# Kernel tuning notes

Measured on AMD Instinct MI355X. Metric: run time of the kernel, lower is better.

## Reference

```python
import jax, jax.numpy as jnp
import numpy as np

K = 3          # k_neighbors
EPS = 1e-12    # F.normalize eps


def _l2norm(x):
    n = jnp.sqrt(jnp.sum(x * x, axis=-1, keepdims=True))
    return x / jnp.maximum(n, EPS)


def setup_inputs() -> dict:
    key = jax.random.key(0)
    k1, k2 = jax.random.split(key)
    query_features = jax.random.normal(k1, (64, 64, 32, 32), dtype=jnp.float32)
    support_features = jax.random.normal(k2, (64, 5, 64, 1024), dtype=jnp.float32)
    return {"query_features": query_features, "support_features": support_features}


def reference(query_features, support_features):
    B, D, h, w = query_features.shape
    # (B, Nq, D), L2-normalized along D
    q_local = _l2norm(query_features.reshape(B, D, h * w).transpose(0, 2, 1))
    # support: (B, Way, D, Ns) -> (B, Way, Ns, D), L2-normalized along D
    s_local = _l2norm(support_features.transpose(0, 1, 3, 2))
    # cosine similarities for all (batch, way) pairs in one batched matmul
    sim = jnp.einsum('bqd,bwsd->bwqs', q_local, s_local)  # (B, Way, Nq, Ns)
    k_actual = min(K, sim.shape[-1])
    topk_sim, _ = jax.lax.top_k(sim, k_actual)            # (B, Way, Nq, k)
    return topk_sim.sum(axis=(-1, -2))                    # (B, Way)
```

## Files before the change

kernel.cpp:

```cpp
#include <hip/hip_runtime.h>
#include <hip/hip_bf16.h>


using bf16x8 = __attribute__((ext_vector_type(8))) short;
using f32x4  = __attribute__((ext_vector_type(4))) float;

__device__ inline unsigned cvt_pk_bf16(float lo, float hi) {
    unsigned r;
    asm("v_cvt_pk_bf16_f32 %0, %1, %2" : "=v"(r) : "v"(lo), "v"(hi));
    return r;
}

__device__ inline uint4 pack8cvt(const float* v) {
    uint4 r;
    r.x = cvt_pk_bf16(v[0], v[1]);
    r.y = cvt_pk_bf16(v[2], v[3]);
    r.z = cvt_pk_bf16(v[4], v[5]);
    r.w = cvt_pk_bf16(v[6], v[7]);
    return r;
}

#define INS(v, T0, T1, T2) do {                         \
    float _v = (v);                                     \
    float _n0 = fmaxf((T0), _v);                        \
    float _n1 = __builtin_amdgcn_fmed3f(_v, (T0), (T1));\
    float _n2 = __builtin_amdgcn_fmed3f(_v, (T1), (T2));\
    (T0) = _n0; (T1) = _n1; (T2) = _n2;                 \
} while (0)

__device__ inline void gload16(const void* g, void* lds) {
    __builtin_amdgcn_global_load_lds(
        (const __attribute__((address_space(1))) unsigned int*)g,
        (__attribute__((address_space(3))) unsigned int*)lds,
        16, 0, 0);
}


__global__ __launch_bounds__(256) void prep_all(const float* __restrict__ Q,
                                                const float* __restrict__ S,
                                                uint4* __restrict__ Qbf,
                                                uint4* __restrict__ Sbf,
                                                float* __restrict__ rnq) {
    const int blk = blockIdx.x;
    if (blk < 256) {
        const int b = blk >> 2;
        const int col = ((blk & 3) << 8) + threadIdx.x;
        const float* p = Q + (size_t)b * 65536 + col;
        float v[64];
        #pragma unroll
        for (int d = 0; d < 64; ++d) v[d] = p[(size_t)d << 10];
        float ss = 0.f;
        #pragma unroll
        for (int d = 0; d < 64; ++d) ss += v[d] * v[d];
        rnq[(b << 10) + col] = 1.0f / fmaxf(sqrtf(ss), 1e-12f);
        uint4* ob = Qbf + ((size_t)(b << 6) + (col >> 4)) * 128 + (col & 15);
        #pragma unroll
        for (int h = 0; h < 8; ++h)
            ob[h << 4] = pack8cvt(&v[h << 3]);
    } else {
        const int bw = (blk - 256) >> 2;
        const int col = ((blk & 3) << 8) + threadIdx.x;
        const float* p = S + (size_t)bw * 65536 + col;
        float v[64];
        #pragma unroll
        for (int d = 0; d < 64; ++d) v[d] = p[(size_t)d << 10];
        float ss = 0.f;
        #pragma unroll
        for (int d = 0; d < 64; ++d) ss += v[d] * v[d];
        const float rs = 1.0f / fmaxf(sqrtf(ss), 1e-12f);
        #pragma unroll
        for (int d = 0; d < 64; ++d) v[d] *= rs;
        uint4* ob = Sbf + ((size_t)(bw << 6) + (col >> 4)) * 128 + (col & 15);
        #pragma unroll
        for (int h = 0; h < 8; ++h)
            ob[h << 4] = pack8cvt(&v[h << 3]);
    }
}

__global__ __launch_bounds__(256) void knn_main(const uint4* __restrict__ Qbf,
                                                const uint4* __restrict__ Sbf,
                                                const float* __restrict__ rnq,
                                                float* __restrict__ partial) {
    __shared__ uint4 ring[8 * 256];
    __shared__ float wsum[4];
    const int lin = blockIdx.x;
    const int l   = (lin & 7) * 160 + (lin >> 3);
    const int qc  = l & 3;
    const int bw  = l >> 2;
    const int b   = bw / 5;
    const int wv = threadIdx.x >> 6, lane = threadIdx.x & 63;

    const uint4* qb = Qbf + ((size_t)(b << 6) + (qc << 4) + (wv << 2)) * 128 + lane;
    bf16x8 bq[4][2];
    #pragma unroll
    for (int qt = 0; qt < 4; ++qt)
        #pragma unroll
        for (int c = 0; c < 2; ++c)
            bq[qt][c] = *reinterpret_cast<const bf16x8*>(&qb[qt * 128 + (c << 6)]);

    const char* sbase = (const char*)(Sbf + (size_t)(bw << 6) * 128);
    const size_t toff = (size_t)threadIdx.x * 16;

    float t0[4], t1[4], t2[4];
    #pragma unroll
    for (int qt = 0; qt < 4; ++qt) { t0[qt] = -1e30f; t1[qt] = -1e30f; t2[qt] = -1e30f; }

    #pragma unroll
    for (int p = 0; p < 4; ++p)
        gload16(sbase + (size_t)p * 4096 + toff, &ring[(p << 8) + (wv << 6)]);

    for (int p = 0; p < 28; ++p) {
        gload16(sbase + (size_t)(p + 4) * 4096 + toff,
                &ring[(((p + 4) & 7) << 8) + (wv << 6)]);
        asm volatile("s_waitcnt vmcnt(4)" ::: "memory");
        __builtin_amdgcn_s_barrier();
        const uint4* sp = &ring[((p & 7) << 8)];
        #pragma unroll
        for (int tt = 0; tt < 2; ++tt) {
            bf16x8 a0 = *reinterpret_cast<const bf16x8*>(&sp[tt * 128 + lane]);
            bf16x8 a1 = *reinterpret_cast<const bf16x8*>(&sp[tt * 128 + 64 + lane]);
            #pragma unroll
            for (int qt = 0; qt < 4; ++qt) {
                f32x4 c = {0.f, 0.f, 0.f, 0.f};
                c = __builtin_amdgcn_mfma_f32_16x16x32_bf16(a0, bq[qt][0], c, 0, 0, 0);
                c = __builtin_amdgcn_mfma_f32_16x16x32_bf16(a1, bq[qt][1], c, 0, 0, 0);
                #pragma unroll
                for (int j = 0; j < 4; ++j)
                    INS(c[j], t0[qt], t1[qt], t2[qt]);
            }
        }
        __builtin_amdgcn_s_barrier();
    }
    asm volatile("s_waitcnt vmcnt(0)" ::: "memory");
    __builtin_amdgcn_s_barrier();
    for (int p = 28; p < 32; ++p) {
        const uint4* sp = &ring[((p & 7) << 8)];
        #pragma unroll
        for (int tt = 0; tt < 2; ++tt) {
            bf16x8 a0 = *reinterpret_cast<const bf16x8*>(&sp[tt * 128 + lane]);
            bf16x8 a1 = *reinterpret_cast<const bf16x8*>(&sp[tt * 128 + 64 + lane]);
            #pragma unroll
            for (int qt = 0; qt < 4; ++qt) {
                f32x4 c = {0.f, 0.f, 0.f, 0.f};
                c = __builtin_amdgcn_mfma_f32_16x16x32_bf16(a0, bq[qt][0], c, 0, 0, 0);
                c = __builtin_amdgcn_mfma_f32_16x16x32_bf16(a1, bq[qt][1], c, 0, 0, 0);
                #pragma unroll
                for (int j = 0; j < 4; ++j)
                    INS(c[j], t0[qt], t1[qt], t2[qt]);
            }
        }
    }

    float s3 = 0.f;
    #pragma unroll
    for (int qt = 0; qt < 4; ++qt) {
        #pragma unroll
        for (int m = 16; m <= 32; m <<= 1) {
            float b0 = __shfl_xor(t0[qt], m);
            float b1 = __shfl_xor(t1[qt], m);
            float b2 = __shfl_xor(t2[qt], m);
            INS(b0, t0[qt], t1[qt], t2[qt]);
            INS(b1, t0[qt], t1[qt], t2[qt]);
            INS(b2, t0[qt], t1[qt], t2[qt]);
        }
        const int qg = (qc << 8) + (wv << 6) + (qt << 4) + (lane & 15);
        s3 += (t0[qt] + t1[qt] + t2[qt]) * rnq[(b << 10) + qg];
    }
    #pragma unroll
    for (int m = 1; m < 64; m <<= 1) s3 += __shfl_xor(s3, m);
    s3 *= 0.25f;
    if (lane == 0) wsum[wv] = s3;
    __syncthreads();
    if (threadIdx.x == 0)
        partial[((size_t)bw << 2) + qc] = (wsum[0] + wsum[1]) + (wsum[2] + wsum[3]);
}

__global__ void finalize4(const float* __restrict__ partial, float* __restrict__ out) {
    int i = blockIdx.x * blockDim.x + threadIdx.x;
    if (i < 320)
        out[i] = (partial[4 * i] + partial[4 * i + 1]) +
                 (partial[4 * i + 2] + partial[4 * i + 3]);
}

__global__ void norms_kernel(const float* __restrict__ Q, const float* __restrict__ S,
                             float* __restrict__ rnq, float* __restrict__ rns) {
    int gid = blockIdx.x * blockDim.x + threadIdx.x;
    if (gid < 65536) {
        int b = gid >> 10, qi = gid & 1023;
        const float* p = Q + (size_t)b * 65536 + qi;
        float ss = 0.f;
        #pragma unroll
        for (int d = 0; d < 64; ++d) { float v = p[(size_t)d * 1024]; ss += v * v; }
        rnq[gid] = 1.0f / fmaxf(sqrtf(ss), 1e-12f);
    } else {
        int v = gid - 65536;
        int bw = v >> 10, si = v & 1023;
        const float* p = S + (size_t)bw * 65536 + si;
        float ss = 0.f;
        #pragma unroll
        for (int d = 0; d < 64; ++d) { float x = p[(size_t)d * 1024]; ss += x * x; }
        rns[v] = 1.0f / fmaxf(sqrtf(ss), 1e-12f);
    }
}

__global__ __launch_bounds__(512, 4) void knn_fb(
        const float* __restrict__ Q, const float* __restrict__ S,
        const float* __restrict__ rnq, const float* __restrict__ rns,
        float* __restrict__ partial) {
    __shared__ uint4 qfrag[16 * 128];
    __shared__ uint4 sfrag[2][4 * 128];
    __shared__ float wsum[8];

    const int qc = blockIdx.x, w = blockIdx.y, b = blockIdx.z;
    const int t = threadIdx.x, wv = t >> 6, lane = t & 63;

    const float* Qb   = Q + (size_t)b * 65536;
    const float* Sb   = S + (size_t)(b * 5 + w) * 65536;
    const float* rnqb = rnq + (b << 10);
    const float* rnsb = rns + ((b * 5 + w) << 10);

    bf16x8 bq[4][2];
    for (int ph = 0; ph < 2; ++ph) {
        for (int sub = 0; sub < 4; ++sub) {
            int qg = (qc << 9) + (ph << 8) + (sub << 6) + lane;
            float v[8];
            #pragma unroll
            for (int i = 0; i < 8; ++i)
                v[i] = Qb[(size_t)((wv << 3) + i) * 1024 + qg];
            qfrag[((sub << 2) + (lane >> 4)) * 128 + (wv << 4) + (lane & 15)] = pack8cvt(v);
        }
        __syncthreads();
        if ((wv >> 2) == ph) {
            #pragma unroll
            for (int qt = 0; qt < 4; ++qt)
                #pragma unroll
                for (int c = 0; c < 2; ++c)
                    bq[qt][c] = *reinterpret_cast<const bf16x8*>(
                        &qfrag[(((wv & 3) << 2) + qt) * 128 + (c << 6) + lane]);
        }
        __syncthreads();
    }

    {
        float sv[8]; float rs = rnsb[lane];
        #pragma unroll
        for (int i = 0; i < 8; ++i)
            sv[i] = Sb[(size_t)((wv << 3) + i) * 1024 + lane] * rs;
        sfrag[0][(lane >> 4) * 128 + (wv << 4) + (lane & 15)] = pack8cvt(sv);
    }
    __syncthreads();

    float t0[4], t1[4], t2[4];
    #pragma unroll
    for (int qt = 0; qt < 4; ++qt) { t0[qt] = -1e30f; t1[qt] = -1e30f; t2[qt] = -1e30f; }
    int cur = 0;
    const float* sp = Sb + ((wv << 3) << 10) + lane;

    for (int blk = 0; blk < 16; ++blk) {
        float sv[8]; float rs;
        if (blk < 15) {
            const int sb_ = (blk + 1) << 6;
            rs = rnsb[sb_ + lane];
            #pragma unroll
            for (int i = 0; i < 8; ++i)
                sv[i] = sp[(size_t)(i << 10) + sb_];
        }
        #pragma unroll
        for (int st = 0; st < 4; ++st) {
            bf16x8 a0 = *reinterpret_cast<const bf16x8*>(&sfrag[cur][st * 128 + lane]);
            bf16x8 a1 = *reinterpret_cast<const bf16x8*>(&sfrag[cur][st * 128 + 64 + lane]);
            #pragma unroll
            for (int qt = 0; qt < 4; ++qt) {
                f32x4 c = {0.f, 0.f, 0.f, 0.f};
                c = __builtin_amdgcn_mfma_f32_16x16x32_bf16(a0, bq[qt][0], c, 0, 0, 0);
                c = __builtin_amdgcn_mfma_f32_16x16x32_bf16(a1, bq[qt][1], c, 0, 0, 0);
                #pragma unroll
                for (int j = 0; j < 4; ++j)
                    INS(c[j], t0[qt], t1[qt], t2[qt]);
            }
        }
        if (blk < 15) {
            #pragma unroll
            for (int i = 0; i < 8; ++i) sv[i] *= rs;
            sfrag[cur ^ 1][(lane >> 4) * 128 + (wv << 4) + (lane & 15)] = pack8cvt(sv);
        }
        __syncthreads();
        cur ^= 1;
    }

    float s3 = 0.f;
    #pragma unroll
    for (int qt = 0; qt < 4; ++qt) {
        #pragma unroll
        for (int m = 16; m <= 32; m <<= 1) {
            float b0 = __shfl_xor(t0[qt], m);
            float b1 = __shfl_xor(t1[qt], m);
            float b2 = __shfl_xor(t2[qt], m);
            INS(b0, t0[qt], t1[qt], t2[qt]);
            INS(b1, t0[qt], t1[qt], t2[qt]);
            INS(b2, t0[qt], t1[qt], t2[qt]);
        }
        int qg = (qc << 9) + (wv << 6) + (qt << 4) + (lane & 15);
        s3 += (t0[qt] + t1[qt] + t2[qt]) * rnqb[qg];
    }
    #pragma unroll
    for (int m = 1; m < 64; m <<= 1) s3 += __shfl_xor(s3, m);
    s3 *= 0.25f;
    if (lane == 0) wsum[wv] = s3;
    __syncthreads();
    if (t == 0) {
        float acc = 0.f;
        #pragma unroll
        for (int i = 0; i < 8; ++i) acc += wsum[i];
        partial[((b * 5 + w) << 1) + qc] = acc;
    }
}

__global__ void finalize2(const float* __restrict__ partial, float* __restrict__ out) {
    int i = blockIdx.x * blockDim.x + threadIdx.x;
    if (i < 320)
        out[i] = partial[2 * i] + partial[2 * i + 1];
}

extern "C" void kernel_launch(void* const* d_in, const int* in_sizes, int n_in,
                              void* d_out, int out_size, void* d_ws, size_t ws_size,
                              hipStream_t stream) {
    const float* Q = (const float*)d_in[0];
    const float* S = (const float*)d_in[1];
    float* out = (float*)d_out;

    const size_t QBF = 8388608ull, SBF = 41943040ull, RNQ = 262144ull;
    const size_t NEED = QBF + SBF + RNQ + 5120ull;
    if (ws_size >= NEED) {
        char* base = (char*)d_ws;
        uint4* Qbf     = (uint4*)base;
        uint4* Sbf     = (uint4*)(base + QBF);
        float* rnq     = (float*)(base + QBF + SBF);
        float* partial = (float*)(base + QBF + SBF + RNQ);
        prep_all<<<1536, 256, 0, stream>>>(Q, S, Qbf, Sbf, rnq);
        knn_main<<<1280, 256, 0, stream>>>(Qbf, Sbf, rnq, partial);
        finalize4<<<2, 256, 0, stream>>>(partial, out);
    } else {
        float* rnq = (float*)d_ws;
        float* rns = rnq + 65536;
        float* partial = rns + 327680;
        norms_kernel<<<(65536 + 327680) / 256, 256, 0, stream>>>(Q, S, rnq, rns);
        knn_fb<<<dim3(2, 5, 64), 512, 0, stream>>>(Q, S, rnq, rns, partial);
        finalize2<<<2, 256, 0, stream>>>(partial, out);
    }
}
```

Baseline: 101.2 us.

## Software-pipeline MFMA tiles with top-k insertion using double accumulators

Result: faster. 92.03 us (-9.1%).

```diff
diff --git a/kernel.cpp b/kernel.cpp
--- a/kernel.cpp
+++ b/kernel.cpp
@@ -77,10 +77,31 @@
     }
 }
 
-__global__ __launch_bounds__(256) void knn_main(const uint4* __restrict__ Qbf,
-                                                const uint4* __restrict__ Sbf,
-                                                const float* __restrict__ rnq,
-                                                float* __restrict__ partial) {
+__device__ __forceinline__ void mfma_tile(const uint4* sp, int lane,
+                                          const bf16x8 (&bq)[4][2],
+                                          const f32x4& fz, f32x4* c) {
+    bf16x8 a0 = *reinterpret_cast<const bf16x8*>(&sp[lane]);
+    bf16x8 a1 = *reinterpret_cast<const bf16x8*>(&sp[64 + lane]);
+    #pragma unroll
+    for (int qt = 0; qt < 4; ++qt) {
+        c[qt] = __builtin_amdgcn_mfma_f32_16x16x32_bf16(a0, bq[qt][0], fz, 0, 0, 0);
+        c[qt] = __builtin_amdgcn_mfma_f32_16x16x32_bf16(a1, bq[qt][1], c[qt], 0, 0, 0);
+    }
+}
+
+__device__ __forceinline__ void ins_tile(const f32x4* c,
+                                         float (&t0)[4], float (&t1)[4], float (&t2)[4]) {
+    #pragma unroll
+    for (int qt = 0; qt < 4; ++qt)
+        #pragma unroll
+        for (int j = 0; j < 4; ++j)
+            INS(c[qt][j], t0[qt], t1[qt], t2[qt]);
+}
+
+__global__ __launch_bounds__(256, 4) void knn_main(const uint4* __restrict__ Qbf,
+                                                   const uint4* __restrict__ Sbf,
+                                                   const float* __restrict__ rnq,
+                                                   float* __restrict__ partial) {
     __shared__ uint4 ring[8 * 256];
     __shared__ float wsum[4];
     const int lin = blockIdx.x;
@@ -98,6 +119,10 @@
         for (int c = 0; c < 2; ++c)
             bq[qt][c] = *reinterpret_cast<const bf16x8*>(&qb[qt * 128 + (c << 6)]);
 
+    float z0 = 0.f;
+    asm volatile("" : "+v"(z0));
+    const f32x4 fz = {z0, z0, z0, z0};
+
     const char* sbase = (const char*)(Sbf + (size_t)(bw << 6) * 128);
     const size_t toff = (size_t)threadIdx.x * 16;
 
@@ -105,51 +130,40 @@
     #pragma unroll
     for (int qt = 0; qt < 4; ++qt) { t0[qt] = -1e30f; t1[qt] = -1e30f; t2[qt] = -1e30f; }
 
+    f32x4 cA[4], cB[4];
+
     #pragma unroll
     for (int p = 0; p < 4; ++p)
         gload16(sbase + (size_t)p * 4096 + toff, &ring[(p << 8) + (wv << 6)]);
 
-    for (int p = 0; p < 28; ++p) {
+    gload16(sbase + 4 * 4096 + toff, &ring[(4 << 8) + (wv << 6)]);
+    asm volatile("s_waitcnt vmcnt(4)" ::: "memory");
+    __builtin_amdgcn_s_barrier();
+    mfma_tile(&ring[0], lane, bq, fz, cA);
+    mfma_tile(&ring[128], lane, bq, fz, cB);
+
+    for (int p = 1; p <= 27; ++p) {
         gload16(sbase + (size_t)(p + 4) * 4096 + toff,
                 &ring[(((p + 4) & 7) << 8) + (wv << 6)]);
         asm volatile("s_waitcnt vmcnt(4)" ::: "memory");
         __builtin_amdgcn_s_barrier();
         const uint4* sp = &ring[((p & 7) << 8)];
-        #pragma unroll
-        for (int tt = 0; tt < 2; ++tt) {
-            bf16x8 a0 = *reinterpret_cast<const bf16x8*>(&sp[tt * 128 + lane]);
-            bf16x8 a1 = *reinterpret_cast<const bf16x8*>(&sp[tt * 128 + 64 + lane]);
-            #pragma unroll
-            for (int qt = 0; qt < 4; ++qt) {
-                f32x4 c = {0.f, 0.f, 0.f, 0.f};
-                c = __builtin_amdgcn_mfma_f32_16x16x32_bf16(a0, bq[qt][0], c, 0, 0, 0);
-                c = __builtin_amdgcn_mfma_f32_16x16x32_bf16(a1, bq[qt][1], c, 0, 0, 0);
-                #pragma unroll
-                for (int j = 0; j < 4; ++j)
-                    INS(c[j], t0[qt], t1[qt], t2[qt]);
-            }
-        }
-        __builtin_amdgcn_s_barrier();
+        mfma_tile(sp, lane, bq, fz, cA);
+        ins_tile(cB, t0, t1, t2);
+        mfma_tile(sp + 128, lane, bq, fz, cB);
+        ins_tile(cA, t0, t1, t2);
     }
     asm volatile("s_waitcnt vmcnt(0)" ::: "memory");
     __builtin_amdgcn_s_barrier();
-    for (int p = 28; p < 32; ++p) {
+    #pragma unroll
+    for (int p = 28; p <= 31; ++p) {
         const uint4* sp = &ring[((p & 7) << 8)];
-        #pragma unroll
-        for (int tt = 0; tt < 2; ++tt) {
-            bf16x8 a0 = *reinterpret_cast<const bf16x8*>(&sp[tt * 128 + lane]);
-            bf16x8 a1 = *reinterpret_cast<const bf16x8*>(&sp[tt * 128 + 64 + lane]);
-            #pragma unroll
-            for (int qt = 0; qt < 4; ++qt) {
-                f32x4 c = {0.f, 0.f, 0.f, 0.f};
-                c = __builtin_amdgcn_mfma_f32_16x16x32_bf16(a0, bq[qt][0], c, 0, 0, 0);
-                c = __builtin_amdgcn_mfma_f32_16x16x32_bf16(a1, bq[qt][1], c, 0, 0, 0);
-                #pragma unroll
-                for (int j = 0; j < 4; ++j)
-                    INS(c[j], t0[qt], t1[qt], t2[qt]);
-            }
-        }
-    }
+        mfma_tile(sp, lane, bq, fz, cA);
+        ins_tile(cB, t0, t1, t2);
+        mfma_tile(sp + 128, lane, bq, fz, cB);
+        ins_tile(cA, t0, t1, t2);
+    }
+    ins_tile(cB, t0, t1, t2);
 
     float s3 = 0.f;
     #pragma unroll
```

## Split query chunks eightfold with staggered support ring and MFMA priority

Applied to the files above, without the earlier changes.

Result: no change. 99.30 us (-1.9%).

```diff
diff --git a/kernel.cpp b/kernel.cpp
--- a/kernel.cpp
+++ b/kernel.cpp
@@ -77,23 +77,47 @@
     }
 }
 
-__global__ __launch_bounds__(256) void knn_main(const uint4* __restrict__ Qbf,
-                                                const uint4* __restrict__ Sbf,
-                                                const float* __restrict__ rnq,
-                                                float* __restrict__ partial) {
-    __shared__ uint4 ring[8 * 256];
+__device__ __forceinline__ void compute_tile(const uint4* sp, int lane,
+                                             const bf16x8 (&bq)[2][2],
+                                             float (&t0)[2], float (&t1)[2],
+                                             float (&t2)[2]) {
+    bf16x8 a0 = *reinterpret_cast<const bf16x8*>(&sp[lane]);
+    bf16x8 a1 = *reinterpret_cast<const bf16x8*>(&sp[64 + lane]);
+    const f32x4 z = {0.f, 0.f, 0.f, 0.f};
+    __builtin_amdgcn_s_setprio(1);
+    f32x4 c0 = __builtin_amdgcn_mfma_f32_16x16x32_bf16(a0, bq[0][0], z, 0, 0, 0);
+    c0 = __builtin_amdgcn_mfma_f32_16x16x32_bf16(a1, bq[0][1], c0, 0, 0, 0);
+    f32x4 c1 = __builtin_amdgcn_mfma_f32_16x16x32_bf16(a0, bq[1][0], z, 0, 0, 0);
+    c1 = __builtin_amdgcn_mfma_f32_16x16x32_bf16(a1, bq[1][1], c1, 0, 0, 0);
+    __builtin_amdgcn_s_setprio(0);
+    INS(c0[0], t0[0], t1[0], t2[0]);
+    INS(c0[1], t0[0], t1[0], t2[0]);
+    INS(c0[2], t0[0], t1[0], t2[0]);
+    INS(c0[3], t0[0], t1[0], t2[0]);
+    INS(c1[0], t0[1], t1[1], t2[1]);
+    INS(c1[1], t0[1], t1[1], t2[1]);
+    INS(c1[2], t0[1], t1[1], t2[1]);
+    INS(c1[3], t0[1], t1[1], t2[1]);
+}
+
+__global__ __launch_bounds__(256, 8) void knn_main(const uint4* __restrict__ Qbf,
+                                                   const uint4* __restrict__ Sbf,
+                                                   const float* __restrict__ rnq,
+                                                   float* __restrict__ partial) {
+    __shared__ uint4 ring[5 * 256];
     __shared__ float wsum[4];
     const int lin = blockIdx.x;
-    const int l   = (lin & 7) * 160 + (lin >> 3);
-    const int qc  = l & 3;
-    const int bw  = l >> 2;
+    const int l   = (lin & 7) * 320 + (lin >> 3);
+    const int qc  = l & 7;
+    const int bw  = l >> 3;
     const int b   = bw / 5;
     const int wv = threadIdx.x >> 6, lane = threadIdx.x & 63;
-
-    const uint4* qb = Qbf + ((size_t)(b << 6) + (qc << 4) + (wv << 2)) * 128 + lane;
-    bf16x8 bq[4][2];
-    #pragma unroll
-    for (int qt = 0; qt < 4; ++qt)
+    const int sp0 = qc << 2;
+
+    const uint4* qb = Qbf + ((size_t)(b << 6) + (qc << 3) + (wv << 1)) * 128 + lane;
+    bf16x8 bq[2][2];
+    #pragma unroll
+    for (int qt = 0; qt < 2; ++qt)
         #pragma unroll
         for (int c = 0; c < 2; ++c)
             bq[qt][c] = *reinterpret_cast<const bf16x8*>(&qb[qt * 128 + (c << 6)]);
@@ -101,24 +125,162 @@
     const char* sbase = (const char*)(Sbf + (size_t)(bw << 6) * 128);
     const size_t toff = (size_t)threadIdx.x * 16;
 
+    float t0[2], t1[2], t2[2];
+    #pragma unroll
+    for (int qt = 0; qt < 2; ++qt) { t0[qt] = -1e30f; t1[qt] = -1e30f; t2[qt] = -1e30f; }
+
+    #pragma unroll
+    for (int p = 0; p < 3; ++p)
+        gload16(sbase + (size_t)((p + sp0) & 31) * 4096 + toff,
+                &ring[(p << 8) + (wv << 6)]);
+
+    int rslot = 0, wslot = 3;
+    for (int p = 0; p <= 28; ++p) {
+        gload16(sbase + (size_t)((p + 3 + sp0) & 31) * 4096 + toff,
+                &ring[(wslot << 8) + (wv << 6)]);
+        asm volatile("s_waitcnt vmcnt(3)" ::: "memory");
+        __builtin_amdgcn_s_barrier();
+        const uint4* sp = &ring[rslot << 8];
+        compute_tile(sp, lane, bq, t0, t1, t2);
+        compute_tile(sp + 128, lane, bq, t0, t1, t2);
+        if (++rslot == 5) rslot = 0;
+        if (++wslot == 5) wslot = 0;
+    }
+    asm volatile("s_waitcnt vmcnt(0)" ::: "memory");
+    __builtin_amdgcn_s_barrier();
+    {
+        const uint4* sp = &ring[4 << 8];
+        compute_tile(sp, lane, bq, t0, t1, t2);
+        compute_tile(sp + 128, lane, bq, t0, t1, t2);
+        sp = &ring[0];
+        compute_tile(sp, lane, bq, t0, t1, t2);
+        compute_tile(sp + 128, lane, bq, t0, t1, t2);
+        sp = &ring[1 << 8];
+        compute_tile(sp, lane, bq, t0, t1, t2);
+        compute_tile(sp + 128, lane, bq, t0, t1, t2);
+    }
+
+    float s3 = 0.f;
+    #pragma unroll
+    for (int qt = 0; qt < 2; ++qt) {
+        #pragma unroll
+        for (int m = 16; m <= 32; m <<= 1) {
+            float b0 = __shfl_xor(t0[qt], m);
+            float b1 = __shfl_xor(t1[qt], m);
+            float b2 = __shfl_xor(t2[qt], m);
+            INS(b0, t0[qt], t1[qt], t2[qt]);
+            INS(b1, t0[qt], t1[qt], t2[qt]);
+            INS(b2, t0[qt], t1[qt], t2[qt]);
+        }
+        const int qg = (qc << 7) + (wv << 5) + (qt << 4) + (lane & 15);
+        s3 += (t0[qt] + t1[qt] + t2[qt]) * rnq[(b << 10) + qg];
+    }
+    #pragma unroll
+    for (int m = 1; m < 64; m <<= 1) s3 += __shfl_xor(s3, m);
+    s3 *= 0.25f;
+    if (lane == 0) wsum[wv] = s3;
+    __syncthreads();
+    if (threadIdx.x == 0)
+        partial[((size_t)bw << 3) + qc] = (wsum[0] + wsum[1]) + (wsum[2] + wsum[3]);
+}
+
+__global__ void finalize8(const float* __restrict__ partial, float* __restrict__ out) {
+    int i = blockIdx.x * blockDim.x + threadIdx.x;
+    if (i < 320) {
+        float a = 0.f;
+        #pragma unroll
+        for (int k = 0; k < 8; ++k) a += partial[8 * i + k];
+        out[i] = a;
+    }
+}
+
+__global__ void norms_kernel(const float* __restrict__ Q, const float* __restrict__ S,
+                             float* __restrict__ rnq, float* __restrict__ rns) {
+    int gid = blockIdx.x * blockDim.x + threadIdx.x;
+    if (gid < 65536) {
+        int b = gid >> 10, qi = gid & 1023;
+        const float* p = Q + (size_t)b * 65536 + qi;
+        float ss = 0.f;
+        #pragma unroll
+        for (int d = 0; d < 64; ++d) { float v = p[(size_t)d * 1024]; ss += v * v; }
+        rnq[gid] = 1.0f / fmaxf(sqrtf(ss), 1e-12f);
+    } else {
+        int v = gid - 65536;
+        int bw = v >> 10, si = v & 1023;
+        const float* p = S + (size_t)bw * 65536 + si;
+        float ss = 0.f;
+        #pragma unroll
+        for (int d = 0; d < 64; ++d) { float x = p[(size_t)d * 1024]; ss += x * x; }
+        rns[v] = 1.0f / fmaxf(sqrtf(ss), 1e-12f);
+    }
+}
+
+__global__ __launch_bounds__(512, 4) void knn_fb(
+        const float* __restrict__ Q, const float* __restrict__ S,
+        const float* __restrict__ rnq, const float* __restrict__ rns,
+        float* __restrict__ partial) {
+    __shared__ uint4 qfrag[16 * 128];
+    __shared__ uint4 sfrag[2][4 * 128];
+    __shared__ float wsum[8];
+
+    const int qc = blockIdx.x, w = blockIdx.y, b = blockIdx.z;
+    const int t = threadIdx.x, wv = t >> 6, lane = t & 63;
+
+    const float* Qb   = Q + (size_t)b * 65536;
+    const float* Sb   = S + (size_t)(b * 5 + w) * 65536;
+    const float* rnqb = rnq + (b << 10);
+    const float* rnsb = rns + ((b * 5 + w) << 10);
+
+    bf16x8 bq[4][2];
+    for (int ph = 0; ph < 2; ++ph) {
+        for (int sub = 0; sub < 4; ++sub) {
+            int qg = (qc << 9) + (ph << 8) + (sub << 6) + lane;
+            float v[8];
+            #pragma unroll
+            for (int i = 0; i < 8; ++i)
+                v[i] = Qb[(size_t)((wv << 3) + i) * 1024 + qg];
+            qfrag[((sub << 2) + (lane >> 4)) * 128 + (wv << 4) + (lane & 15)] = pack8cvt(v);
+        }
+        __syncthreads();
+        if ((wv >> 2) == ph) {
+            #pragma unroll
+            for (int qt = 0; qt < 4; ++qt)
+                #pragma unroll
+                for (int c = 0; c < 2; ++c)
+                    bq[qt][c] = *reinterpret_cast<const bf16x8*>(
+                        &qfrag[(((wv & 3) << 2) + qt) * 128 + (c << 6) + lane]);
+        }
+        __syncthreads();
+    }
+
+    {
+        float sv[8]; float rs = rnsb[lane];
+        #pragma unroll
+        for (int i = 0; i < 8; ++i)
+            sv[i] = Sb[(size_t)((wv << 3) + i) * 1024 + lane] * rs;
+        sfrag[0][(lane >> 4) * 128 + (wv << 4) + (lane & 15)] = pack8cvt(sv);
+    }
+    __syncthreads();
+
     float t0[4], t1[4], t2[4];
     #pragma unroll
     for (int qt = 0; qt < 4; ++qt) { t0[qt] = -1e30f; t1[qt] = -1e30f; t2[qt] = -1e30f; }
-
-    #pragma unroll
-    for (int p = 0; p < 4; ++p)
-        gload16(sbase + (size_t)p * 4096 + toff, &ring[(p << 8) + (wv << 6)]);
-
-    for (int p = 0; p < 28; ++p) {
-        gload16(sbase + (size_t)(p + 4) * 4096 + toff,
-                &ring[(((p + 4) & 7) << 8) + (wv << 6)]);
-        asm volatile("s_waitcnt vmcnt(4)" ::: "memory");
-        __builtin_amdgcn_s_barrier();
-        const uint4* sp = &ring[((p & 7) << 8)];
-        #pragma unroll
-        for (int tt = 0; tt < 2; ++tt) {
-            bf16x8 a0 = *reinterpret_cast<const bf16x8*>(&sp[tt * 128 + lane]);
-            bf16x8 a1 = *reinterpret_cast<const bf16x8*>(&sp[tt * 128 + 64 + lane]);
+    int cur = 0;
+    const float* sp = Sb + ((wv << 3) << 10) + lane;
+
+    for (int blk = 0; blk < 16; ++blk) {
+        float sv[8]; float rs;
+        if (blk < 15) {
+            const int sb_ = (blk + 1) << 6;
+            rs = rnsb[sb_ + lane];
+            #pragma unroll
+            for (int i = 0; i < 8; ++i)
+                sv[i] = sp[(size_t)(i << 10) + sb_];
+        }
+        #pragma unroll
+        for (int st = 0; st < 4; ++st) {
+            bf16x8 a0 = *reinterpret_cast<const bf16x8*>(&sfrag[cur][st * 128 + lane]);
+            bf16x8 a1 = *reinterpret_cast<const bf16x8*>(&sfrag[cur][st * 128 + 64 + lane]);
             #pragma unroll
             for (int qt = 0; qt < 4; ++qt) {
                 f32x4 c = {0.f, 0.f, 0.f, 0.f};
@@ -129,26 +291,13 @@
                     INS(c[j], t0[qt], t1[qt], t2[qt]);
             }
         }
-        __builtin_amdgcn_s_barrier();
-    }
-    asm volatile("s_waitcnt vmcnt(0)" ::: "memory");
-    __builtin_amdgcn_s_barrier();
-    for (int p = 28; p < 32; ++p) {
-        const uint4* sp = &ring[((p & 7) << 8)];
-        #pragma unroll
-        for (int tt = 0; tt < 2; ++tt) {
-            bf16x8 a0 = *reinterpret_cast<const bf16x8*>(&sp[tt * 128 + lane]);
-            bf16x8 a1 = *reinterpret_cast<const bf16x8*>(&sp[tt * 128 + 64 + lane]);
-            #pragma unroll
-            for (int qt = 0; qt < 4; ++qt) {
-                f32x4 c = {0.f, 0.f, 0.f, 0.f};
-                c = __builtin_amdgcn_mfma_f32_16x16x32_bf16(a0, bq[qt][0], c, 0, 0, 0);
-                c = __builtin_amdgcn_mfma_f32_16x16x32_bf16(a1, bq[qt][1], c, 0, 0, 0);
-                #pragma unroll
-                for (int j = 0; j < 4; ++j)
-                    INS(c[j], t0[qt], t1[qt], t2[qt]);
-            }
-        }
+        if (blk < 15) {
+            #pragma unroll
+            for (int i = 0; i < 8; ++i) sv[i] *= rs;
+            sfrag[cur ^ 1][(lane >> 4) * 128 + (wv << 4) + (lane & 15)] = pack8cvt(sv);
+        }
+        __syncthreads();
+        cur ^= 1;
     }
 
     float s3 = 0.f;
@@ -163,143 +312,6 @@
             INS(b1, t0[qt], t1[qt], t2[qt]);
             INS(b2, t0[qt], t1[qt], t2[qt]);
         }
-        const int qg = (qc << 8) + (wv << 6) + (qt << 4) + (lane & 15);
-        s3 += (t0[qt] + t1[qt] + t2[qt]) * rnq[(b << 10) + qg];
-    }
-    #pragma unroll
-    for (int m = 1; m < 64; m <<= 1) s3 += __shfl_xor(s3, m);
-    s3 *= 0.25f;
-    if (lane == 0) wsum[wv] = s3;
-    __syncthreads();
-    if (threadIdx.x == 0)
-        partial[((size_t)bw << 2) + qc] = (wsum[0] + wsum[1]) + (wsum[2] + wsum[3]);
-}
-
-__global__ void finalize4(const float* __restrict__ partial, float* __restrict__ out) {
-    int i = blockIdx.x * blockDim.x + threadIdx.x;
-    if (i < 320)
-        out[i] = (partial[4 * i] + partial[4 * i + 1]) +
-                 (partial[4 * i + 2] + partial[4 * i + 3]);
-}
-
-__global__ void norms_kernel(const float* __restrict__ Q, const float* __restrict__ S,
-                             float* __restrict__ rnq, float* __restrict__ rns) {
-    int gid = blockIdx.x * blockDim.x + threadIdx.x;
-    if (gid < 65536) {
-        int b = gid >> 10, qi = gid & 1023;
-        const float* p = Q + (size_t)b * 65536 + qi;
-        float ss = 0.f;
-        #pragma unroll
-        for (int d = 0; d < 64; ++d) { float v = p[(size_t)d * 1024]; ss += v * v; }
-        rnq[gid] = 1.0f / fmaxf(sqrtf(ss), 1e-12f);
-    } else {
-        int v = gid - 65536;
-        int bw = v >> 10, si = v & 1023;
-        const float* p = S + (size_t)bw * 65536 + si;
-        float ss = 0.f;
-        #pragma unroll
-        for (int d = 0; d < 64; ++d) { float x = p[(size_t)d * 1024]; ss += x * x; }
-        rns[v] = 1.0f / fmaxf(sqrtf(ss), 1e-12f);
-    }
-}
-
-__global__ __launch_bounds__(512, 4) void knn_fb(
-        const float* __restrict__ Q, const float* __restrict__ S,
-        const float* __restrict__ rnq, const float* __restrict__ rns,
-        float* __restrict__ partial) {
-    __shared__ uint4 qfrag[16 * 128];
-    __shared__ uint4 sfrag[2][4 * 128];
-    __shared__ float wsum[8];
-
-    const int qc = blockIdx.x, w = blockIdx.y, b = blockIdx.z;
-    const int t = threadIdx.x, wv = t >> 6, lane = t & 63;
-
-    const float* Qb   = Q + (size_t)b * 65536;
-    const float* Sb   = S + (size_t)(b * 5 + w) * 65536;
-    const float* rnqb = rnq + (b << 10);
-    const float* rnsb = rns + ((b * 5 + w) << 10);
-
-    bf16x8 bq[4][2];
-    for (int ph = 0; ph < 2; ++ph) {
-        for (int sub = 0; sub < 4; ++sub) {
-            int qg = (qc << 9) + (ph << 8) + (sub << 6) + lane;
-            float v[8];
-            #pragma unroll
-            for (int i = 0; i < 8; ++i)
-                v[i] = Qb[(size_t)((wv << 3) + i) * 1024 + qg];
-            qfrag[((sub << 2) + (lane >> 4)) * 128 + (wv << 4) + (lane & 15)] = pack8cvt(v);
-        }
-        __syncthreads();
-        if ((wv >> 2) == ph) {
-            #pragma unroll
-            for (int qt = 0; qt < 4; ++qt)
-                #pragma unroll
-                for (int c = 0; c < 2; ++c)
-                    bq[qt][c] = *reinterpret_cast<const bf16x8*>(
-                        &qfrag[(((wv & 3) << 2) + qt) * 128 + (c << 6) + lane]);
-        }
-        __syncthreads();
-    }
-
-    {
-        float sv[8]; float rs = rnsb[lane];
-        #pragma unroll
-        for (int i = 0; i < 8; ++i)
-            sv[i] = Sb[(size_t)((wv << 3) + i) * 1024 + lane] * rs;
-        sfrag[0][(lane >> 4) * 128 + (wv << 4) + (lane & 15)] = pack8cvt(sv);
-    }
-    __syncthreads();
-
-    float t0[4], t1[4], t2[4];
-    #pragma unroll
-    for (int qt = 0; qt < 4; ++qt) { t0[qt] = -1e30f; t1[qt] = -1e30f; t2[qt] = -1e30f; }
-    int cur = 0;
-    const float* sp = Sb + ((wv << 3) << 10) + lane;
-
-    for (int blk = 0; blk < 16; ++blk) {
-        float sv[8]; float rs;
-        if (blk < 15) {
-            const int sb_ = (blk + 1) << 6;
-            rs = rnsb[sb_ + lane];
-            #pragma unroll
-            for (int i = 0; i < 8; ++i)
-                sv[i] = sp[(size_t)(i << 10) + sb_];
-        }
-        #pragma unroll
-        for (int st = 0; st < 4; ++st) {
-            bf16x8 a0 = *reinterpret_cast<const bf16x8*>(&sfrag[cur][st * 128 + lane]);
-            bf16x8 a1 = *reinterpret_cast<const bf16x8*>(&sfrag[cur][st * 128 + 64 + lane]);
-            #pragma unroll
-            for (int qt = 0; qt < 4; ++qt) {
-                f32x4 c = {0.f, 0.f, 0.f, 0.f};
-                c = __builtin_amdgcn_mfma_f32_16x16x32_bf16(a0, bq[qt][0], c, 0, 0, 0);
-                c = __builtin_amdgcn_mfma_f32_16x16x32_bf16(a1, bq[qt][1], c, 0, 0, 0);
-                #pragma unroll
-                for (int j = 0; j < 4; ++j)
-                    INS(c[j], t0[qt], t1[qt], t2[qt]);
-            }
-        }
-        if (blk < 15) {
-            #pragma unroll
-            for (int i = 0; i < 8; ++i) sv[i] *= rs;
-            sfrag[cur ^ 1][(lane >> 4) * 128 + (wv << 4) + (lane & 15)] = pack8cvt(sv);
-        }
-        __syncthreads();
-        cur ^= 1;
-    }
-
-    float s3 = 0.f;
-    #pragma unroll
-    for (int qt = 0; qt < 4; ++qt) {
-        #pragma unroll
-        for (int m = 16; m <= 32; m <<= 1) {
-            float b0 = __shfl_xor(t0[qt], m);
-            float b1 = __shfl_xor(t1[qt], m);
-            float b2 = __shfl_xor(t2[qt], m);
-            INS(b0, t0[qt], t1[qt], t2[qt]);
-            INS(b1, t0[qt], t1[qt], t2[qt]);
-            INS(b2, t0[qt], t1[qt], t2[qt]);
-        }
         int qg = (qc << 9) + (wv << 6) + (qt << 4) + (lane & 15);
         s3 += (t0[qt] + t1[qt] + t2[qt]) * rnqb[qg];
     }
@@ -330,7 +342,7 @@
     float* out = (float*)d_out;
 
     const size_t QBF = 8388608ull, SBF = 41943040ull, RNQ = 262144ull;
-    const size_t NEED = QBF + SBF + RNQ + 5120ull;
+    const size_t NEED = QBF + SBF + RNQ + 10240ull;
     if (ws_size >= NEED) {
         char* base = (char*)d_ws;
         uint4* Qbf     = (uint4*)base;
@@ -338,8 +350,8 @@
         float* rnq     = (float*)(base + QBF + SBF);
         float* partial = (float*)(base + QBF + SBF + RNQ);
         prep_all<<<1536, 256, 0, stream>>>(Q, S, Qbf, Sbf, rnq);
-        knn_main<<<1280, 256, 0, stream>>>(Qbf, Sbf, rnq, partial);
-        finalize4<<<2, 256, 0, stream>>>(partial, out);
+        knn_main<<<2560, 256, 0, stream>>>(Qbf, Sbf, rnq, partial);
+        finalize8<<<2, 256, 0, stream>>>(partial, out);
     } else {
         float* rnq = (float*)d_ws;
         float* rns = rnq + 65536;
```

## Split support columns across wave pairs with per-wave LDS rings, no block barriers

Applied to the files above, without the earlier changes.

Measured after the change: 95.42 us. 1.06x faster.

```diff
diff --git a/kernel.cpp b/kernel.cpp
--- a/kernel.cpp
+++ b/kernel.cpp
@@ -77,20 +77,44 @@
     }
 }
 
-__global__ __launch_bounds__(256) void knn_main(const uint4* __restrict__ Qbf,
-                                                const uint4* __restrict__ Sbf,
-                                                const float* __restrict__ rnq,
-                                                float* __restrict__ partial) {
-    __shared__ uint4 ring[8 * 256];
-    __shared__ float wsum[4];
+__device__ __forceinline__ void compute_tile4(const uint4* sp, int lane,
+                                              const bf16x8 (&bq)[4][2],
+                                              float (&t0)[4], float (&t1)[4],
+                                              float (&t2)[4]) {
+    bf16x8 a0 = *reinterpret_cast<const bf16x8*>(&sp[lane]);
+    bf16x8 a1 = *reinterpret_cast<const bf16x8*>(&sp[64 + lane]);
+    const f32x4 z = {0.f, 0.f, 0.f, 0.f};
+    f32x4 c[4];
+    __builtin_amdgcn_s_setprio(1);
+    #pragma unroll
+    for (int qt = 0; qt < 4; ++qt) {
+        c[qt] = __builtin_amdgcn_mfma_f32_16x16x32_bf16(a0, bq[qt][0], z, 0, 0, 0);
+        c[qt] = __builtin_amdgcn_mfma_f32_16x16x32_bf16(a1, bq[qt][1], c[qt], 0, 0, 0);
+    }
+    __builtin_amdgcn_s_setprio(0);
+    #pragma unroll
+    for (int qt = 0; qt < 4; ++qt) {
+        INS(c[qt][0], t0[qt], t1[qt], t2[qt]);
+        INS(c[qt][1], t0[qt], t1[qt], t2[qt]);
+        INS(c[qt][2], t0[qt], t1[qt], t2[qt]);
+        INS(c[qt][3], t0[qt], t1[qt], t2[qt]);
+    }
+}
+
+__global__ __launch_bounds__(256, 4) void knn_main(const uint4* __restrict__ Qbf,
+                                                   const uint4* __restrict__ Sbf,
+                                                   const float* __restrict__ rnq,
+                                                   float* __restrict__ partial) {
+    __shared__ uint4 ring[4][5 * 128];
     const int lin = blockIdx.x;
-    const int l   = (lin & 7) * 160 + (lin >> 3);
-    const int qc  = l & 3;
-    const int bw  = l >> 2;
+    const int l   = (lin & 7) * 320 + (lin >> 3);
+    const int qc  = l & 7;
+    const int bw  = l >> 3;
     const int b   = bw / 5;
     const int wv = threadIdx.x >> 6, lane = threadIdx.x & 63;
-
-    const uint4* qb = Qbf + ((size_t)(b << 6) + (qc << 4) + (wv << 2)) * 128 + lane;
+    const int g  = wv >> 1, h = wv & 1;
+
+    const uint4* qb = Qbf + ((size_t)(b << 6) + (qc << 3) + (g << 2)) * 128 + lane;
     bf16x8 bq[4][2];
     #pragma unroll
     for (int qt = 0; qt < 4; ++qt)
@@ -98,27 +122,179 @@
         for (int c = 0; c < 2; ++c)
             bq[qt][c] = *reinterpret_cast<const bf16x8*>(&qb[qt * 128 + (c << 6)]);
 
-    const char* sbase = (const char*)(Sbf + (size_t)(bw << 6) * 128);
-    const size_t toff = (size_t)threadIdx.x * 16;
+    const char* sbyte = (const char*)(Sbf + (size_t)bw * 8192) + ((size_t)h << 16)
+                        + (size_t)lane * 16;
+    uint4* myring = &ring[wv][0];
 
     float t0[4], t1[4], t2[4];
     #pragma unroll
     for (int qt = 0; qt < 4; ++qt) { t0[qt] = -1e30f; t1[qt] = -1e30f; t2[qt] = -1e30f; }
 
     #pragma unroll
-    for (int p = 0; p < 4; ++p)
-        gload16(sbase + (size_t)p * 4096 + toff, &ring[(p << 8) + (wv << 6)]);
-
-    for (int p = 0; p < 28; ++p) {
-        gload16(sbase + (size_t)(p + 4) * 4096 + toff,
-                &ring[(((p + 4) & 7) << 8) + (wv << 6)]);
-        asm volatile("s_waitcnt vmcnt(4)" ::: "memory");
-        __builtin_amdgcn_s_barrier();
-        const uint4* sp = &ring[((p & 7) << 8)];
-        #pragma unroll
-        for (int tt = 0; tt < 2; ++tt) {
-            bf16x8 a0 = *reinterpret_cast<const bf16x8*>(&sp[tt * 128 + lane]);
-            bf16x8 a1 = *reinterpret_cast<const bf16x8*>(&sp[tt * 128 + 64 + lane]);
+    for (int t = 0; t < 3; ++t) {
+        gload16(sbyte + (size_t)t * 2048,        &myring[t * 128]);
+        gload16(sbyte + (size_t)t * 2048 + 1024, &myring[t * 128 + 64]);
+    }
+
+    int rslot = 0, wslot = 3;
+    for (int t = 0; t <= 28; ++t) {
+        gload16(sbyte + (size_t)(t + 3) * 2048,        &myring[wslot * 128]);
+        gload16(sbyte + (size_t)(t + 3) * 2048 + 1024, &myring[wslot * 128 + 64]);
+        asm volatile("s_waitcnt vmcnt(6)" ::: "memory");
+        compute_tile4(&myring[rslot * 128], lane, bq, t0, t1, t2);
+        if (++rslot == 5) rslot = 0;
+        if (++wslot == 5) wslot = 0;
+    }
+    asm volatile("s_waitcnt vmcnt(4)" ::: "memory");
+    compute_tile4(&myring[4 * 128], lane, bq, t0, t1, t2);
+    asm volatile("s_waitcnt vmcnt(2)" ::: "memory");
+    compute_tile4(&myring[0], lane, bq, t0, t1, t2);
+    asm volatile("s_waitcnt vmcnt(0)" ::: "memory");
+    compute_tile4(&myring[1 * 128], lane, bq, t0, t1, t2);
+
+    #pragma unroll
+    for (int qt = 0; qt < 4; ++qt) {
+        #pragma unroll
+        for (int m = 16; m <= 32; m <<= 1) {
+            float b0 = __shfl_xor(t0[qt], m);
+            float b1 = __shfl_xor(t1[qt], m);
+            float b2 = __shfl_xor(t2[qt], m);
+            INS(b0, t0[qt], t1[qt], t2[qt]);
+            INS(b1, t0[qt], t1[qt], t2[qt]);
+            INS(b2, t0[qt], t1[qt], t2[qt]);
+        }
+    }
+
+    if (h == 1) {
+        float* tb = (float*)&ring[wv][0];
+        if (lane < 16) {
+            #pragma unroll
+            for (int qt = 0; qt < 4; ++qt) {
+                tb[qt * 48 + lane]      = t0[qt];
+                tb[qt * 48 + 16 + lane] = t1[qt];
+                tb[qt * 48 + 32 + lane] = t2[qt];
+            }
+        }
+    }
+    __syncthreads();
+    if (h == 0) {
+        const float* tb = (const float*)&ring[wv + 1][0];
+        float s3 = 0.f;
+        #pragma unroll
+        for (int qt = 0; qt < 4; ++qt) {
+            float u0 = tb[qt * 48 + (lane & 15)];
+            float u1 = tb[qt * 48 + 16 + (lane & 15)];
+            float u2 = tb[qt * 48 + 32 + (lane & 15)];
+            INS(u0, t0[qt], t1[qt], t2[qt]);
+            INS(u1, t0[qt], t1[qt], t2[qt]);
+            INS(u2, t0[qt], t1[qt], t2[qt]);
+            const int qg = (qc << 7) + (g << 6) + (qt << 4) + (lane & 15);
+            s3 += (t0[qt] + t1[qt] + t2[qt]) * rnq[(b << 10) + qg];
+        }
+        #pragma unroll
+        for (int m = 1; m < 64; m <<= 1) s3 += __shfl_xor(s3, m);
+        s3 *= 0.25f;
+        if (lane == 0) partial[(size_t)bw * 16 + qc * 2 + g] = s3;
+    }
+}
+
+__global__ void finalize16(const float* __restrict__ partial, float* __restrict__ out) {
+    int i = blockIdx.x * blockDim.x + threadIdx.x;
+    if (i < 320) {
+        float a = 0.f;
+        #pragma unroll
+        for (int k = 0; k < 16; ++k) a += partial[16 * i + k];
+        out[i] = a;
+    }
+}
+
+__global__ void norms_kernel(const float* __restrict__ Q, const float* __restrict__ S,
+                             float* __restrict__ rnq, float* __restrict__ rns) {
+    int gid = blockIdx.x * blockDim.x + threadIdx.x;
+    if (gid < 65536) {
+        int b = gid >> 10, qi = gid & 1023;
+        const float* p = Q + (size_t)b * 65536 + qi;
+        float ss = 0.f;
+        #pragma unroll
+        for (int d = 0; d < 64; ++d) { float v = p[(size_t)d * 1024]; ss += v * v; }
+        rnq[gid] = 1.0f / fmaxf(sqrtf(ss), 1e-12f);
+    } else {
+        int v = gid - 65536;
+        int bw = v >> 10, si = v & 1023;
+        const float* p = S + (size_t)bw * 65536 + si;
+        float ss = 0.f;
+        #pragma unroll
+        for (int d = 0; d < 64; ++d) { float x = p[(size_t)d * 1024]; ss += x * x; }
+        rns[v] = 1.0f / fmaxf(sqrtf(ss), 1e-12f);
+    }
+}
+
+__global__ __launch_bounds__(512, 4) void knn_fb(
+        const float* __restrict__ Q, const float* __restrict__ S,
+        const float* __restrict__ rnq, const float* __restrict__ rns,
+        float* __restrict__ partial) {
+    __shared__ uint4 qfrag[16 * 128];
+    __shared__ uint4 sfrag[2][4 * 128];
+    __shared__ float wsum[8];
+
+    const int qc = blockIdx.x, w = blockIdx.y, b = blockIdx.z;
+    const int t = threadIdx.x, wv = t >> 6, lane = t & 63;
+
+    const float* Qb   = Q + (size_t)b * 65536;
+    const float* Sb   = S + (size_t)(b * 5 + w) * 65536;
+    const float* rnqb = rnq + (b << 10);
+    const float* rnsb = rns + ((b * 5 + w) << 10);
+
+    bf16x8 bq[4][2];
+    for (int ph = 0; ph < 2; ++ph) {
+        for (int sub = 0; sub < 4; ++sub) {
+            int qg = (qc << 9) + (ph << 8) + (sub << 6) + lane;
+            float v[8];
+            #pragma unroll
+            for (int i = 0; i < 8; ++i)
+                v[i] = Qb[(size_t)((wv << 3) + i) * 1024 + qg];
+            qfrag[((sub << 2) + (lane >> 4)) * 128 + (wv << 4) + (lane & 15)] = pack8cvt(v);
+        }
+        __syncthreads();
+        if ((wv >> 2) == ph) {
+            #pragma unroll
+            for (int qt = 0; qt < 4; ++qt)
+                #pragma unroll
+                for (int c = 0; c < 2; ++c)
+                    bq[qt][c] = *reinterpret_cast<const bf16x8*>(
+                        &qfrag[(((wv & 3) << 2) + qt) * 128 + (c << 6) + lane]);
+        }
+        __syncthreads();
+    }
+
+    {
+        float sv[8]; float rs = rnsb[lane];
+        #pragma unroll
+        for (int i = 0; i < 8; ++i)
+            sv[i] = Sb[(size_t)((wv << 3) + i) * 1024 + lane] * rs;
+        sfrag[0][(lane >> 4) * 128 + (wv << 4) + (lane & 15)] = pack8cvt(sv);
+    }
+    __syncthreads();
+
+    float t0[4], t1[4], t2[4];
+    #pragma unroll
+    for (int qt = 0; qt < 4; ++qt) { t0[qt] = -1e30f; t1[qt] = -1e30f; t2[qt] = -1e30f; }
+    int cur = 0;
+    const float* sp = Sb + ((wv << 3) << 10) + lane;
+
+    for (int blk = 0; blk < 16; ++blk) {
+        float sv[8]; float rs;
+        if (blk < 15) {
+            const int sb_ = (blk + 1) << 6;
+            rs = rnsb[sb_ + lane];
+            #pragma unroll
+            for (int i = 0; i < 8; ++i)
+                sv[i] = sp[(size_t)(i << 10) + sb_];
+        }
+        #pragma unroll
+        for (int st = 0; st < 4; ++st) {
+            bf16x8 a0 = *reinterpret_cast<const bf16x8*>(&sfrag[cur][st * 128 + lane]);
+            bf16x8 a1 = *reinterpret_cast<const bf16x8*>(&sfrag[cur][st * 128 + 64 + lane]);
             #pragma unroll
             for (int qt = 0; qt < 4; ++qt) {
                 f32x4 c = {0.f, 0.f, 0.f, 0.f};
@@ -129,26 +305,13 @@
                     INS(c[j], t0[qt], t1[qt], t2[qt]);
             }
         }
-        __builtin_amdgcn_s_barrier();
-    }
-    asm volatile("s_waitcnt vmcnt(0)" ::: "memory");
-    __builtin_amdgcn_s_barrier();
-    for (int p = 28; p < 32; ++p) {
-        const uint4* sp = &ring[((p & 7) << 8)];
-        #pragma unroll
-        for (int tt = 0; tt < 2; ++tt) {
-            bf16x8 a0 = *reinterpret_cast<const bf16x8*>(&sp[tt * 128 + lane]);
-            bf16x8 a1 = *reinterpret_cast<const bf16x8*>(&sp[tt * 128 + 64 + lane]);
-            #pragma unroll
-            for (int qt = 0; qt < 4; ++qt) {
-                f32x4 c = {0.f, 0.f, 0.f, 0.f};
-                c = __builtin_amdgcn_mfma_f32_16x16x32_bf16(a0, bq[qt][0], c, 0, 0, 0);
-                c = __builtin_amdgcn_mfma_f32_16x16x32_bf16(a1, bq[qt][1], c, 0, 0, 0);
-                #pragma unroll
-                for (int j = 0; j < 4; ++j)
-                    INS(c[j], t0[qt], t1[qt], t2[qt]);
-            }
-        }
+        if (blk < 15) {
+            #pragma unroll
+            for (int i = 0; i < 8; ++i) sv[i] *= rs;
+            sfrag[cur ^ 1][(lane >> 4) * 128 + (wv << 4) + (lane & 15)] = pack8cvt(sv);
+        }
+        __syncthreads();
+        cur ^= 1;
     }
 
     float s3 = 0.f;
@@ -163,143 +326,6 @@
             INS(b1, t0[qt], t1[qt], t2[qt]);
             INS(b2, t0[qt], t1[qt], t2[qt]);
         }
-        const int qg = (qc << 8) + (wv << 6) + (qt << 4) + (lane & 15);
-        s3 += (t0[qt] + t1[qt] + t2[qt]) * rnq[(b << 10) + qg];
-    }
-    #pragma unroll
-    for (int m = 1; m < 64; m <<= 1) s3 += __shfl_xor(s3, m);
-    s3 *= 0.25f;
-    if (lane == 0) wsum[wv] = s3;
-    __syncthreads();
-    if (threadIdx.x == 0)
-        partial[((size_t)bw << 2) + qc] = (wsum[0] + wsum[1]) + (wsum[2] + wsum[3]);
-}
-
-__global__ void finalize4(const float* __restrict__ partial, float* __restrict__ out) {
-    int i = blockIdx.x * blockDim.x + threadIdx.x;
-    if (i < 320)
-        out[i] = (partial[4 * i] + partial[4 * i + 1]) +
-                 (partial[4 * i + 2] + partial[4 * i + 3]);
-}
-
-__global__ void norms_kernel(const float* __restrict__ Q, const float* __restrict__ S,
-                             float* __restrict__ rnq, float* __restrict__ rns) {
-    int gid = blockIdx.x * blockDim.x + threadIdx.x;
-    if (gid < 65536) {
-        int b = gid >> 10, qi = gid & 1023;
-        const float* p = Q + (size_t)b * 65536 + qi;
-        float ss = 0.f;
-        #pragma unroll
-        for (int d = 0; d < 64; ++d) { float v = p[(size_t)d * 1024]; ss += v * v; }
-        rnq[gid] = 1.0f / fmaxf(sqrtf(ss), 1e-12f);
-    } else {
-        int v = gid - 65536;
-        int bw = v >> 10, si = v & 1023;
-        const float* p = S + (size_t)bw * 65536 + si;
-        float ss = 0.f;
-        #pragma unroll
-        for (int d = 0; d < 64; ++d) { float x = p[(size_t)d * 1024]; ss += x * x; }
-        rns[v] = 1.0f / fmaxf(sqrtf(ss), 1e-12f);
-    }
-}
-
-__global__ __launch_bounds__(512, 4) void knn_fb(
-        const float* __restrict__ Q, const float* __restrict__ S,
-        const float* __restrict__ rnq, const float* __restrict__ rns,
-        float* __restrict__ partial) {
-    __shared__ uint4 qfrag[16 * 128];
-    __shared__ uint4 sfrag[2][4 * 128];
-    __shared__ float wsum[8];
-
-    const int qc = blockIdx.x, w = blockIdx.y, b = blockIdx.z;
-    const int t = threadIdx.x, wv = t >> 6, lane = t & 63;
-
-    const float* Qb   = Q + (size_t)b * 65536;
-    const float* Sb   = S + (size_t)(b * 5 + w) * 65536;
-    const float* rnqb = rnq + (b << 10);
-    const float* rnsb = rns + ((b * 5 + w) << 10);
-
-    bf16x8 bq[4][2];
-    for (int ph = 0; ph < 2; ++ph) {
-        for (int sub = 0; sub < 4; ++sub) {
-            int qg = (qc << 9) + (ph << 8) + (sub << 6) + lane;
-            float v[8];
-            #pragma unroll
-            for (int i = 0; i < 8; ++i)
-                v[i] = Qb[(size_t)((wv << 3) + i) * 1024 + qg];
-            qfrag[((sub << 2) + (lane >> 4)) * 128 + (wv << 4) + (lane & 15)] = pack8cvt(v);
-        }
-        __syncthreads();
-        if ((wv >> 2) == ph) {
-            #pragma unroll
-            for (int qt = 0; qt < 4; ++qt)
-                #pragma unroll
-                for (int c = 0; c < 2; ++c)
-                    bq[qt][c] = *reinterpret_cast<const bf16x8*>(
-                        &qfrag[(((wv & 3) << 2) + qt) * 128 + (c << 6) + lane]);
-        }
-        __syncthreads();
-    }
-
-    {
-        float sv[8]; float rs = rnsb[lane];
-        #pragma unroll
-        for (int i = 0; i < 8; ++i)
-            sv[i] = Sb[(size_t)((wv << 3) + i) * 1024 + lane] * rs;
-        sfrag[0][(lane >> 4) * 128 + (wv << 4) + (lane & 15)] = pack8cvt(sv);
-    }
-    __syncthreads();
-
-    float t0[4], t1[4], t2[4];
-    #pragma unroll
-    for (int qt = 0; qt < 4; ++qt) { t0[qt] = -1e30f; t1[qt] = -1e30f; t2[qt] = -1e30f; }
-    int cur = 0;
-    const float* sp = Sb + ((wv << 3) << 10) + lane;
-
-    for (int blk = 0; blk < 16; ++blk) {
-        float sv[8]; float rs;
-        if (blk < 15) {
-            const int sb_ = (blk + 1) << 6;
-            rs = rnsb[sb_ + lane];
-            #pragma unroll
-            for (int i = 0; i < 8; ++i)
-                sv[i] = sp[(size_t)(i << 10) + sb_];
-        }
-        #pragma unroll
-        for (int st = 0; st < 4; ++st) {
-            bf16x8 a0 = *reinterpret_cast<const bf16x8*>(&sfrag[cur][st * 128 + lane]);
-            bf16x8 a1 = *reinterpret_cast<const bf16x8*>(&sfrag[cur][st * 128 + 64 + lane]);
-            #pragma unroll
-            for (int qt = 0; qt < 4; ++qt) {
-                f32x4 c = {0.f, 0.f, 0.f, 0.f};
-                c = __builtin_amdgcn_mfma_f32_16x16x32_bf16(a0, bq[qt][0], c, 0, 0, 0);
-                c = __builtin_amdgcn_mfma_f32_16x16x32_bf16(a1, bq[qt][1], c, 0, 0, 0);
-                #pragma unroll
-                for (int j = 0; j < 4; ++j)
-                    INS(c[j], t0[qt], t1[qt], t2[qt]);
-            }
-        }
-        if (blk < 15) {
-            #pragma unroll
-            for (int i = 0; i < 8; ++i) sv[i] *= rs;
-            sfrag[cur ^ 1][(lane >> 4) * 128 + (wv << 4) + (lane & 15)] = pack8cvt(sv);
-        }
-        __syncthreads();
-        cur ^= 1;
-    }
-
-    float s3 = 0.f;
-    #pragma unroll
-    for (int qt = 0; qt < 4; ++qt) {
-        #pragma unroll
-        for (int m = 16; m <= 32; m <<= 1) {
-            float b0 = __shfl_xor(t0[qt], m);
-            float b1 = __shfl_xor(t1[qt], m);
-            float b2 = __shfl_xor(t2[qt], m);
-            INS(b0, t0[qt], t1[qt], t2[qt]);
-            INS(b1, t0[qt], t1[qt], t2[qt]);
-            INS(b2, t0[qt], t1[qt], t2[qt]);
-        }
         int qg = (qc << 9) + (wv << 6) + (qt << 4) + (lane & 15);
         s3 += (t0[qt] + t1[qt] + t2[qt]) * rnqb[qg];
     }
@@ -330,7 +356,7 @@
     float* out = (float*)d_out;
 
     const size_t QBF = 8388608ull, SBF = 41943040ull, RNQ = 262144ull;
-    const size_t NEED = QBF + SBF + RNQ + 5120ull;
+    const size_t NEED = QBF + SBF + RNQ + 20480ull;
     if (ws_size >= NEED) {
         char* base = (char*)d_ws;
         uint4* Qbf     = (uint4*)base;
@@ -338,8 +364,8 @@
         float* rnq     = (float*)(base + QBF + SBF);
         float* partial = (float*)(base + QBF + SBF + RNQ);
         prep_all<<<1536, 256, 0, stream>>>(Q, S, Qbf, Sbf, rnq);
-        knn_main<<<1280, 256, 0, stream>>>(Qbf, Sbf, rnq, partial);
-        finalize4<<<2, 256, 0, stream>>>(partial, out);
+        knn_main<<<2560, 256, 0, stream>>>(Qbf, Sbf, rnq, partial);
+        finalize16<<<2, 256, 0, stream>>>(partial, out);
     } else {
         float* rnq = (float*)d_ws;
         float* rns = rnq + 65536;
```
